# Kernel tuning notes

Hardware: AMD Instinct MI355X
Metric: run time of the kernel (lower is better)

## Reference

```python
import jax, jax.numpy as jnp
import numpy as np

H, A, S, P = 16, 768, 384, 128
D = A // H
B, N = 1, 768

def _ln(x, w=None, b=None, eps=1e-5):
    m = jnp.mean(x, axis=-1, keepdims=True)
    v = jnp.var(x, axis=-1, keepdims=True)
    y = (x - m) * jax.lax.rsqrt(v + eps)
    if w is not None:
        y = y * w
    if b is not None:
        y = y + b
    return y

def setup_inputs() -> dict:
    key = jax.random.key(0)
    ks = jax.random.split(key, 20)
    def rn(k, shape, scale=0.02):
        return jax.random.normal(k, shape, dtype=jnp.float32) * scale
    return {
        'a': jax.random.normal(ks[0], (B, N, A), dtype=jnp.float32),
        's': jax.random.normal(ks[1], (B, N, S), dtype=jnp.float32),
        'pair_rep': jax.random.normal(ks[2], (B, N, N, P), dtype=jnp.float32),
        'beta': jax.random.normal(ks[3], (B, N, N), dtype=jnp.float32),
        # AdaLN params (LN(a) no affine; LN(s) scale-only; sigmoid-gate Linear w/ bias; shift Linear no bias)
        'ln_s_w': jnp.ones((S,), jnp.float32),
        'gamma_w': rn(ks[4], (S, A)), 'gamma_b': jnp.zeros((A,), jnp.float32),
        'shift_w': rn(ks[5], (S, A)),
        # QKV
        'Wq': rn(ks[6], (A, H * D)), 'bq': jnp.zeros((H * D,), jnp.float32),
        'Wk': rn(ks[7], (A, H * D)),
        'Wv': rn(ks[8], (A, H * D)),
        # pair bias: LN + Linear(P -> H, no bias)
        'ln_p_w': jnp.ones((P,), jnp.float32), 'ln_p_b': jnp.zeros((P,), jnp.float32),
        'Wb': rn(ks[9], (P, H)),
        # gate
        'Wg': rn(ks[10], (A, H * D)),
        # output projections
        'Wp': rn(ks[11], (H * D, A)),
        'Wout': rn(ks[12], (S, A)), 'bout': jnp.full((A,), -2.0, jnp.float32),
    }

def reference(a, s, pair_rep, beta, ln_s_w, gamma_w, gamma_b, shift_w, Wq, bq, Wk, Wv, ln_p_w, ln_p_b, Wb, Wg, Wp, Wout, bout):
    # AdaLN(a, s)
    a_n = _ln(a)
    s_n = _ln(s, ln_s_w)
    a2 = jax.nn.sigmoid(s_n @ gamma_w + gamma_b) * a_n + s_n @ shift_w
    # QKV + gate, viewed as [B, N, H, D]
    q = (a2 @ Wq + bq).reshape(B, N, H, D)
    k = (a2 @ Wk).reshape(B, N, H, D)
    v = (a2 @ Wv).reshape(B, N, H, D)
    g = jax.nn.sigmoid((a2 @ Wg).reshape(B, N, H, D))
    # pair bias -> [B, H, N, N]
    bias = _ln(pair_rep, ln_p_w, ln_p_b) @ Wb          # [B, N, N, H]
    bias = bias + beta[..., None]
    bias = jnp.moveaxis(bias, -1, -3)                  # [B, H, N, N]
    # attention
    scores = jnp.einsum('bqhd,bkhd->bhqk', q, k) / np.sqrt(D).astype(np.float32) + bias
    attn = jax.nn.softmax(scores, axis=-1)
    o = jnp.einsum('bhqk,bkhd->bqhd', attn, v) * g     # [B, N, H, D]
    out = o.reshape(B, N, H * D) @ Wp                  # [B, N, A]
    out = jax.nn.sigmoid(s @ Wout + bout) * out
    return out
```

## Files before the change

kernel.cpp:

```cpp
#include <hip/hip_runtime.h>

#define N_ 768
#define S_ 384
#define H_ 16
#define D_ 48
#define P_ 128
#define NN_ (768*768)

typedef __attribute__((ext_vector_type(8))) short bf16x8;
typedef __attribute__((ext_vector_type(4))) float f32x4;

__device__ __forceinline__ unsigned short f2bf(float x) {
  unsigned int u = __float_as_uint(x);
  u = (u + 0x7fffu + ((u >> 16) & 1u)) >> 16;
  return (unsigned short)u;
}
__device__ __forceinline__ float bf2f(unsigned short h) {
  return __uint_as_float(((unsigned int)h) << 16);
}
__device__ __forceinline__ float sigm(float x) { return 1.f / (1.f + __expf(-x)); }

__global__ __launch_bounds__(256) void k_ln_prep(
    const float* __restrict__ a, const float* __restrict__ s,
    const float* __restrict__ ln_s_w, const float* __restrict__ bq,
    const float* __restrict__ ln_p_w, const float* __restrict__ ln_p_b,
    const float* __restrict__ Wb,
    float* __restrict__ a_n,
    unsigned short* __restrict__ s_n_hi, unsigned short* __restrict__ s_n_lo,
    unsigned short* __restrict__ s_hi, unsigned short* __restrict__ s_lo,
    float* __restrict__ bq4, float* __restrict__ Wprime, float* __restrict__ c12)
{
  int b = blockIdx.x;
  int t = threadIdx.x;
  if (b == N_) {
    for (int j = t; j < 3072; j += 256) bq4[j] = (j < 768) ? bq[j] : 0.f;
    for (int idx = t; idx < 2048; idx += 256) Wprime[idx] = ln_p_w[idx >> 4] * Wb[idx];
    if (t < 16) {
      float c1 = 0.f, c2 = 0.f;
      for (int p = 0; p < 128; ++p) { float wb = Wb[p*16 + t]; c1 += ln_p_w[p]*wb; c2 += ln_p_b[p]*wb; }
      c12[t] = c1; c12[16+t] = c2;
    }
    return;
  }
  __shared__ float red[16];
  int w = t >> 6, l = t & 63;
  float v0 = a[b*N_ + t], v1 = a[b*N_ + 256 + t], v2 = a[b*N_ + 512 + t];
  float sm = v0+v1+v2, sq = v0*v0 + v1*v1 + v2*v2;
  #pragma unroll
  for (int o = 32; o; o >>= 1) { sm += __shfl_xor(sm, o); sq += __shfl_xor(sq, o); }
  if (l == 0) { red[w] = sm; red[8+w] = sq; }
  __syncthreads();
  float Sa = red[0]+red[1]+red[2]+red[3];
  float Qa = red[8]+red[9]+red[10]+red[11];
  float mean = Sa * (1.f/768.f);
  float var  = Qa * (1.f/768.f) - mean*mean;
  float inv  = rsqrtf(var + 1e-5f);
  a_n[b*N_ + t]       = (v0-mean)*inv;
  a_n[b*N_ + 256 + t] = (v1-mean)*inv;
  a_n[b*N_ + 512 + t] = (v2-mean)*inv;
  __syncthreads();
  float u0 = s[b*S_ + t];
  float u1 = (t < 128) ? s[b*S_ + 256 + t] : 0.f;
  float sm2 = u0+u1, sq2 = u0*u0 + u1*u1;
  #pragma unroll
  for (int o = 32; o; o >>= 1) { sm2 += __shfl_xor(sm2, o); sq2 += __shfl_xor(sq2, o); }
  if (l == 0) { red[w] = sm2; red[8+w] = sq2; }
  __syncthreads();
  float Ss = red[0]+red[1]+red[2]+red[3];
  float Qs = red[8]+red[9]+red[10]+red[11];
  float means = Ss * (1.f/384.f);
  float vars  = Qs * (1.f/384.f) - means*means;
  float invs  = rsqrtf(vars + 1e-5f);
  {
    float sn = (u0 - means)*invs*ln_s_w[t];
    unsigned short h = f2bf(sn); s_n_hi[b*S_+t] = h; s_n_lo[b*S_+t] = f2bf(sn - bf2f(h));
    unsigned short hr = f2bf(u0); s_hi[b*S_+t] = hr; s_lo[b*S_+t] = f2bf(u0 - bf2f(hr));
  }
  if (t < 128) {
    int c = 256 + t;
    float sn = (u1 - means)*invs*ln_s_w[c];
    unsigned short h = f2bf(sn); s_n_hi[b*S_+c] = h; s_n_lo[b*S_+c] = f2bf(sn - bf2f(h));
    unsigned short hr = f2bf(u1); s_hi[b*S_+c] = hr; s_lo[b*S_+c] = f2bf(u1 - bf2f(hr));
  }
}

struct TDesc { const float* src; unsigned short* hi; unsigned short* lo; int R; int C; };
struct TArgs { TDesc d[8]; };
__global__ __launch_bounds__(256) void k_transpose(TArgs args)
{
  TDesc dd = args.d[blockIdx.z];
  int c0 = blockIdx.x * 32, r0 = blockIdx.y * 32;
  if (r0 >= dd.R || c0 >= dd.C) return;
  __shared__ float tile[32][33];
  int tx = threadIdx.x & 31, ty = threadIdx.x >> 5;
  #pragma unroll
  for (int p = 0; p < 4; ++p) {
    int r = ty + p*8;
    tile[r][tx] = dd.src[(r0 + r)*dd.C + c0 + tx];
  }
  __syncthreads();
  #pragma unroll
  for (int p = 0; p < 4; ++p) {
    int r = ty + p*8;
    float x = tile[tx][r];
    unsigned short h = f2bf(x);
    int oidx = (c0 + r)*dd.R + r0 + tx;
    dd.hi[oidx] = h; dd.lo[oidx] = f2bf(x - bf2f(h));
  }
}

__global__ __launch_bounds__(256) void k_pair_bias(
    const float* __restrict__ pair, const float* __restrict__ beta,
    const float* __restrict__ Wprime, const float* __restrict__ c12,
    float* __restrict__ bias3)
{
  __shared__ float xbuf[4][128];
  int b = blockIdx.x;
  int i = b >> 1, j0 = (b & 1) * 384;
  int t = threadIdx.x, w = t >> 6, l = t & 63;
  int h = l & 15, pg = l >> 4;
  float wreg[32];
  #pragma unroll
  for (int e = 0; e < 32; ++e) wreg[e] = Wprime[(pg*32 + e)*16 + h];
  float c1 = c12[h], c2 = c12[16 + h];
  for (int j = j0 + w; j < j0 + 384; j += 4) {
    const float* px = pair + ((long)i*N_ + j)*P_;
    float2 x2 = *(const float2*)(px + 2*l);
    *(float2*)&xbuf[w][2*l] = x2;
    float sm = x2.x + x2.y, sq = x2.x*x2.x + x2.y*x2.y;
    #pragma unroll
    for (int o = 32; o; o >>= 1) { sm += __shfl_xor(sm, o); sq += __shfl_xor(sq, o); }
    float mean = sm * (1.f/128.f);
    float var  = sq * (1.f/128.f) - mean*mean;
    float inv  = rsqrtf(var + 1e-5f);
    float acc = 0.f;
    #pragma unroll
    for (int e4 = 0; e4 < 8; ++e4) {
      float4 xv = *(const float4*)&xbuf[w][pg*32 + e4*4];
      acc = fmaf(xv.x, wreg[e4*4+0], acc);
      acc = fmaf(xv.y, wreg[e4*4+1], acc);
      acc = fmaf(xv.z, wreg[e4*4+2], acc);
      acc = fmaf(xv.w, wreg[e4*4+3], acc);
    }
    acc += __shfl_xor(acc, 16);
    acc += __shfl_xor(acc, 32);
    float outv = inv*acc - inv*mean*c1 + c2 + beta[(long)i*N_ + j];
    if (pg == 0) bias3[(long)h*NN_ + (long)i*N_ + j] = outv;
  }
}

struct GemmArgs {
  const unsigned short* Ah; const unsigned short* Al;
  const unsigned short* Bh; const unsigned short* Bl;
  int lda, ldb, K;
  long sAz, sBz;
  float* C; int ldc; long sCz;
  const float* aux0; const float* aux1;
  unsigned short* oHi; unsigned short* oLo;
  float scale;
};

template<int WTM, int WTN, bool SPLIT, int EPI>
__global__ __launch_bounds__(256) void k_gemm(GemmArgs g)
{
  constexpr int BM = 2*WTM*16, BN = 2*WTN*16;
  int z = blockIdx.z;
  int m0 = blockIdx.x * BM, n0 = blockIdx.y * BN;
  int t = threadIdx.x, l = t & 63, w = t >> 6;
  int wm = (w >> 1)*(WTM*16), wn = (w & 1)*(WTN*16);
  int r = l & 15, kg = (l >> 4)*8;
  const unsigned short* Ah = g.Ah + (long)z*g.sAz;
  const unsigned short* Bh = g.Bh + (long)z*g.sBz;
  const unsigned short* Al = nullptr; const unsigned short* Bl = nullptr;
  if constexpr (SPLIT) { Al = g.Al + (long)z*g.sAz; Bl = g.Bl + (long)z*g.sBz; }
  f32x4 acc[WTM][WTN] = {};
  for (int k0 = 0; k0 < g.K; k0 += 32) {
    bf16x8 ah[WTM], bh[WTN], al[WTM], bl[WTN];
    #pragma unroll
    for (int mt = 0; mt < WTM; ++mt) {
      long off = (long)(m0 + wm + mt*16 + r)*g.lda + k0 + kg;
      ah[mt] = *(const bf16x8*)(Ah + off);
      if constexpr (SPLIT) al[mt] = *(const bf16x8*)(Al + off);
    }
    #pragma unroll
    for (int nt = 0; nt < WTN; ++nt) {
      long off = (long)(n0 + wn + nt*16 + r)*g.ldb + k0 + kg;
      bh[nt] = *(const bf16x8*)(Bh + off);
      if constexpr (SPLIT) bl[nt] = *(const bf16x8*)(Bl + off);
    }
    #pragma unroll
    for (int mt = 0; mt < WTM; ++mt) {
      #pragma unroll
      for (int nt = 0; nt < WTN; ++nt) {
        acc[mt][nt] = __builtin_amdgcn_mfma_f32_16x16x32_bf16(ah[mt], bh[nt], acc[mt][nt], 0, 0, 0);
        if constexpr (SPLIT) {
          acc[mt][nt] = __builtin_amdgcn_mfma_f32_16x16x32_bf16(al[mt], bh[nt], acc[mt][nt], 0, 0, 0);
          acc[mt][nt] = __builtin_amdgcn_mfma_f32_16x16x32_bf16(ah[mt], bl[nt], acc[mt][nt], 0, 0, 0);
        }
      }
    }
  }
  int rb = (l >> 4)*4, cl = l & 15;
  #pragma unroll
  for (int mt = 0; mt < WTM; ++mt)
  #pragma unroll
  for (int nt = 0; nt < WTN; ++nt)
  #pragma unroll
  for (int ri = 0; ri < 4; ++ri) {
    int row = m0 + wm + mt*16 + rb + ri;
    int col = n0 + wn + nt*16 + cl;
    float v = acc[mt][nt][ri];
    if constexpr (EPI == 0) {
      g.C[(long)z*g.sCz + (long)row*g.ldc + col] = v;
    } else if constexpr (EPI == 1) {
      g.C[(long)row*g.ldc + col] = v + g.aux0[col];
    } else if constexpr (EPI == 2) {
      g.C[(long)z*g.sCz + (long)row*g.ldc + col] =
          v*g.scale + g.aux0[(long)z*NN_ + (long)row*N_ + col];
    } else if constexpr (EPI == 3) {
      if (col < D_) {
        long oidx = (long)row*N_ + z*D_ + col;
        float val = v * g.aux0[oidx];
        unsigned short hh = f2bf(val);
        g.oHi[oidx] = hh; g.oLo[oidx] = f2bf(val - bf2f(hh));
      }
    } else if constexpr (EPI == 4) {
      float sgv = sigm(v + g.aux1[col]);
      long oidx = (long)row*g.ldc + col;
      g.C[oidx] = sgv * g.aux0[oidx];
    }
  }
}

__global__ __launch_bounds__(256) void k_a2(
    const float* __restrict__ gs, const float* __restrict__ gamma_b,
    const float* __restrict__ a_n,
    unsigned short* __restrict__ a2h, unsigned short* __restrict__ a2l)
{
  int i = blockIdx.x;
  int j = blockIdx.y*256 + threadIdx.x;
  float val = sigm(gs[(long)i*1536 + j] + gamma_b[j]) * a_n[(long)i*N_ + j]
            + gs[(long)i*1536 + 768 + j];
  unsigned short h = f2bf(val);
  long idx = (long)i*N_ + j;
  a2h[idx] = h; a2l[idx] = f2bf(val - bf2f(h));
}

__global__ __launch_bounds__(256) void k_qkvg_post(
    const float* __restrict__ qkvg,
    unsigned short* __restrict__ qp, unsigned short* __restrict__ kp,
    unsigned short* __restrict__ vt, float* __restrict__ gg)
{
  int b = blockIdx.x;
  int t = threadIdx.x;
  if (b < N_) {
    long i = b;
    #pragma unroll
    for (int e = 0; e < 4; ++e) {
      int c = t + e*256;
      int h = c >> 6, d = c & 63;
      float qv = (d < D_) ? qkvg[i*3072 + h*D_ + d] : 0.f;
      float kv = (d < D_) ? qkvg[i*3072 + 768 + h*D_ + d] : 0.f;
      qp[i*1024 + c] = f2bf(qv);
      kp[i*1024 + c] = f2bf(kv);
    }
    #pragma unroll
    for (int e = 0; e < 3; ++e) {
      int c = t + e*256;
      gg[i*N_ + c] = sigm(qkvg[i*3072 + 2304 + c]);
    }
  } else {
    __shared__ float tile[64][49];
    int b2 = b - N_;
    int h = b2 / 12, i0 = (b2 % 12) * 64;
    #pragma unroll
    for (int e = 0; e < 12; ++e) {
      int idx = t + e*256;
      int il = idx / 48, d = idx % 48;
      tile[il][d] = qkvg[(long)(i0+il)*3072 + 1536 + h*D_ + d];
    }
    __syncthreads();
    #pragma unroll
    for (int e = 0; e < 12; ++e) {
      int idx = t + e*256;
      int d = idx >> 6, il = idx & 63;
      vt[(long)h*49152 + (long)d*N_ + i0 + il] = f2bf(tile[il][d]);
    }
  }
}

__global__ __launch_bounds__(256) void k_softmax(
    const float* __restrict__ scores, unsigned short* __restrict__ attn)
{
  int row = blockIdx.x*4 + (threadIdx.x >> 6);
  int l = threadIdx.x & 63;
  const float* src = scores + (long)row*N_;
  float x[12];
  #pragma unroll
  for (int e = 0; e < 12; ++e) x[e] = src[l + e*64];
  float m = x[0];
  #pragma unroll
  for (int e = 1; e < 12; ++e) m = fmaxf(m, x[e]);
  #pragma unroll
  for (int o = 32; o; o >>= 1) m = fmaxf(m, __shfl_xor(m, o));
  float ssum = 0.f;
  #pragma unroll
  for (int e = 0; e < 12; ++e) { x[e] = __expf(x[e] - m); ssum += x[e]; }
  #pragma unroll
  for (int o = 32; o; o >>= 1) ssum += __shfl_xor(ssum, o);
  float invs = 1.f / ssum;
  unsigned short* dst = attn + (long)row*N_;
  #pragma unroll
  for (int e = 0; e < 12; ++e) dst[l + e*64] = f2bf(x[e]*invs);
}

extern "C" void kernel_launch(void* const* d_in, const int* in_sizes, int n_in,
                              void* d_out, int out_size, void* d_ws, size_t ws_size,
                              hipStream_t stream) {
  const float* a      = (const float*)d_in[0];
  const float* s      = (const float*)d_in[1];
  const float* pair   = (const float*)d_in[2];
  const float* beta   = (const float*)d_in[3];
  const float* ln_s_w = (const float*)d_in[4];
  const float* gamma_w= (const float*)d_in[5];
  const float* gamma_b= (const float*)d_in[6];
  const float* shift_w= (const float*)d_in[7];
  const float* Wq     = (const float*)d_in[8];
  const float* bq     = (const float*)d_in[9];
  const float* Wk     = (const float*)d_in[10];
  const float* Wv     = (const float*)d_in[11];
  const float* ln_p_w = (const float*)d_in[12];
  const float* ln_p_b = (const float*)d_in[13];
  const float* Wb     = (const float*)d_in[14];
  const float* Wg     = (const float*)d_in[15];
  const float* Wp     = (const float*)d_in[16];
  const float* Wout   = (const float*)d_in[17];
  const float* bout   = (const float*)d_in[18];
  float* out = (float*)d_out;
  (void)in_sizes; (void)n_in; (void)out_size; (void)ws_size;

  char* ws = (char*)d_ws;
  size_t off = 0;
  auto alloc = [&](size_t bytes) -> char* {
    char* p = ws + off;
    off = (off + bytes + 255) & ~(size_t)255;
    return p;
  };
  float* bias3   = (float*)alloc((size_t)H_*NN_*4);
  float* scores  = (float*)alloc((size_t)H_*NN_*4);
  unsigned short* W4T_hi  = (unsigned short*)alloc((size_t)3072*768*2);
  unsigned short* W4T_lo  = (unsigned short*)alloc((size_t)3072*768*2);
  unsigned short* gsT_hi  = (unsigned short*)alloc((size_t)1536*384*2);
  unsigned short* gsT_lo  = (unsigned short*)alloc((size_t)1536*384*2);
  unsigned short* WpT_hi  = (unsigned short*)alloc((size_t)768*768*2);
  unsigned short* WpT_lo  = (unsigned short*)alloc((size_t)768*768*2);
  unsigned short* WoT_hi  = (unsigned short*)alloc((size_t)768*384*2);
  unsigned short* WoT_lo  = (unsigned short*)alloc((size_t)768*384*2);
  float* a_n     = (float*)alloc((size_t)N_*N_*4);
  unsigned short* s_n_hi = (unsigned short*)alloc((size_t)N_*S_*2);
  unsigned short* s_n_lo = (unsigned short*)alloc((size_t)N_*S_*2);
  unsigned short* s_hi   = (unsigned short*)alloc((size_t)N_*S_*2);
  unsigned short* s_lo   = (unsigned short*)alloc((size_t)N_*S_*2);
  float* bq4     = (float*)alloc(3072*4);
  float* Wprime  = (float*)alloc(128*16*4);
  float* c12     = (float*)alloc(32*4);
  unsigned short* a2_hi  = (unsigned short*)alloc((size_t)N_*N_*2);
  unsigned short* a2_lo  = (unsigned short*)alloc((size_t)N_*N_*2);
  float* qkvg    = (float*)alloc((size_t)N_*3072*4);
  unsigned short* qp = (unsigned short*)alloc((size_t)N_*1024*2);
  unsigned short* kp = (unsigned short*)alloc((size_t)N_*1024*2);
  unsigned short* vt = (unsigned short*)alloc((size_t)H_*64*N_*2);
  float* gate    = (float*)alloc((size_t)N_*N_*4);
  float* gs = qkvg;
  unsigned short* attn = (unsigned short*)bias3;
  unsigned short* o_hi = (unsigned short*)scores;
  unsigned short* o_lo = (unsigned short*)((char*)scores + (size_t)N_*N_*2);
  float* out1 = (float*)((char*)scores + (size_t)N_*N_*4);

  dim3 blk(256);

  k_ln_prep<<<dim3(N_ + 1), blk, 0, stream>>>(a, s, ln_s_w, bq, ln_p_w, ln_p_b, Wb,
      a_n, s_n_hi, s_n_lo, s_hi, s_lo, bq4, Wprime, c12);

  TArgs ta;
  ta.d[0] = {gamma_w, gsT_hi,               gsT_lo,               384, 768};
  ta.d[1] = {shift_w, gsT_hi + 768*384,     gsT_lo + 768*384,     384, 768};
  ta.d[2] = {Wq,      W4T_hi,               W4T_lo,               768, 768};
  ta.d[3] = {Wk,      W4T_hi + 1*768*768,   W4T_lo + 1*768*768,   768, 768};
  ta.d[4] = {Wv,      W4T_hi + 2*768*768,   W4T_lo + 2*768*768,   768, 768};
  ta.d[5] = {Wg,      W4T_hi + 3*768*768,   W4T_lo + 3*768*768,   768, 768};
  ta.d[6] = {Wp,      WpT_hi,               WpT_lo,               768, 768};
  ta.d[7] = {Wout,    WoT_hi,               WoT_lo,               384, 768};
  k_transpose<<<dim3(24, 24, 8), blk, 0, stream>>>(ta);

  k_pair_bias<<<dim3(1536), blk, 0, stream>>>(pair, beta, Wprime, c12, bias3);

  GemmArgs g1{};
  g1.Ah = s_n_hi; g1.Al = s_n_lo; g1.Bh = gsT_hi; g1.Bl = gsT_lo;
  g1.lda = 384; g1.ldb = 384; g1.K = 384; g1.C = gs; g1.ldc = 1536;
  k_gemm<4,4,true,0><<<dim3(6,12,1), blk, 0, stream>>>(g1);

  k_a2<<<dim3(768,3), blk, 0, stream>>>(gs, gamma_b, a_n, a2_hi, a2_lo);

  GemmArgs g2{};
  g2.Ah = a2_hi; g2.Al = a2_lo; g2.Bh = W4T_hi; g2.Bl = W4T_lo;
  g2.lda = 768; g2.ldb = 768; g2.K = 768; g2.C = qkvg; g2.ldc = 3072; g2.aux0 = bq4;
  k_gemm<4,4,true,1><<<dim3(6,24,1), blk, 0, stream>>>(g2);

  k_qkvg_post<<<dim3(960), blk, 0, stream>>>(qkvg, qp, kp, vt, gate);

  GemmArgs g3{};
  g3.Ah = qp; g3.Bh = kp; g3.lda = 1024; g3.ldb = 1024; g3.K = 64;
  g3.sAz = 64; g3.sBz = 64; g3.C = scores; g3.ldc = 768; g3.sCz = NN_;
  g3.aux0 = bias3; g3.scale = 0.14433756729740643f;
  k_gemm<4,4,false,2><<<dim3(6,6,16), blk, 0, stream>>>(g3);

  k_softmax<<<dim3(3072), blk, 0, stream>>>(scores, attn);

  GemmArgs g4{};
  g4.Ah = attn; g4.Bh = vt; g4.lda = 768; g4.ldb = 768; g4.K = 768;
  g4.sAz = NN_; g4.sBz = 64*768; g4.aux0 = gate; g4.oHi = o_hi; g4.oLo = o_lo;
  k_gemm<4,2,false,3><<<dim3(6,1,16), blk, 0, stream>>>(g4);

  GemmArgs g5{};
  g5.Ah = o_hi; g5.Al = o_lo; g5.Bh = WpT_hi; g5.Bl = WpT_lo;
  g5.lda = 768; g5.ldb = 768; g5.K = 768; g5.C = out1; g5.ldc = 768;
  k_gemm<4,4,true,0><<<dim3(6,6,1), blk, 0, stream>>>(g5);

  GemmArgs g6{};
  g6.Ah = s_hi; g6.Al = s_lo; g6.Bh = WoT_hi; g6.Bl = WoT_lo;
  g6.lda = 384; g6.ldb = 384; g6.K = 384; g6.C = out; g6.ldc = 768;
  g6.aux0 = out1; g6.aux1 = bout;
  k_gemm<4,4,true,4><<<dim3(6,6,1), blk, 0, stream>>>(g6);
}
```

Measured before the change: 829.7 us.

## Move pair-bias projection onto MFMA and shrink GEMM tiles for more blocks

The pair-bias kernel now computes the LayerNorm'd 128->16 projection with bf16 MFMA instructions, using a hi/lo split of both weights and activations to keep near-fp32 accuracy. This replaces the per-lane scalar FMA loop and shared-memory staging. Separately, all dense GEMM launches switch to smaller warp tiles with proportionally larger grids so more blocks fill the 256 CUs. Smaller tiles give less data reuse per block and more redundant operand loads.

```diff
diff --git a/kernel.cpp b/kernel.cpp
--- a/kernel.cpp
+++ b/kernel.cpp
@@ -19,6 +19,22 @@
   return __uint_as_float(((unsigned int)h) << 16);
 }
 __device__ __forceinline__ float sigm(float x) { return 1.f / (1.f + __expf(-x)); }
+
+__device__ __forceinline__ void split8(const float4& a, const float4& b,
+                                       bf16x8& hi, bf16x8& lo) {
+  float xs[8] = {a.x, a.y, a.z, a.w, b.x, b.y, b.z, b.w};
+  union { bf16x8 v; unsigned int u[4]; } Hh, Ll;
+  #pragma unroll
+  for (int i = 0; i < 4; ++i) {
+    unsigned int u0 = __float_as_uint(xs[2*i]);
+    unsigned int u1 = __float_as_uint(xs[2*i+1]);
+    float l0 = xs[2*i]   - __uint_as_float(u0 & 0xFFFF0000u);
+    float l1 = xs[2*i+1] - __uint_as_float(u1 & 0xFFFF0000u);
+    Hh.u[i] = (u0 >> 16) | (u1 & 0xFFFF0000u);
+    Ll.u[i] = (unsigned int)f2bf(l0) | ((unsigned int)f2bf(l1) << 16);
+  }
+  hi = Hh.v; lo = Ll.v;
+}
 
 __global__ __launch_bounds__(256) void k_ln_prep(
     const float* __restrict__ a, const float* __restrict__ s,
@@ -28,13 +44,22 @@
     float* __restrict__ a_n,
     unsigned short* __restrict__ s_n_hi, unsigned short* __restrict__ s_n_lo,
     unsigned short* __restrict__ s_hi, unsigned short* __restrict__ s_lo,
-    float* __restrict__ bq4, float* __restrict__ Wprime, float* __restrict__ c12)
+    float* __restrict__ bq4,
+    unsigned short* __restrict__ wT_hi, unsigned short* __restrict__ wT_lo,
+    float* __restrict__ c12)
 {
   int b = blockIdx.x;
   int t = threadIdx.x;
   if (b == N_) {
     for (int j = t; j < 3072; j += 256) bq4[j] = (j < 768) ? bq[j] : 0.f;
-    for (int idx = t; idx < 2048; idx += 256) Wprime[idx] = ln_p_w[idx >> 4] * Wb[idx];
+    for (int idx = t; idx < 2048; idx += 256) {
+      int p = idx & 127, h = idx >> 7;
+      float w = ln_p_w[p] * Wb[p*16 + h];
+      unsigned int u = __float_as_uint(w);
+      float lo = w - __uint_as_float(u & 0xFFFF0000u);
+      wT_hi[h*128 + p] = (unsigned short)(u >> 16);
+      wT_lo[h*128 + p] = f2bf(lo);
+    }
     if (t < 16) {
       float c1 = 0.f, c2 = 0.f;
       for (int p = 0; p < 128; ++p) { float wb = Wb[p*16 + t]; c1 += ln_p_w[p]*wb; c2 += ln_p_b[p]*wb; }
@@ -111,41 +136,57 @@
 
 __global__ __launch_bounds__(256) void k_pair_bias(
     const float* __restrict__ pair, const float* __restrict__ beta,
-    const float* __restrict__ Wprime, const float* __restrict__ c12,
-    float* __restrict__ bias3)
-{
-  __shared__ float xbuf[4][128];
-  int b = blockIdx.x;
-  int i = b >> 1, j0 = (b & 1) * 384;
-  int t = threadIdx.x, w = t >> 6, l = t & 63;
-  int h = l & 15, pg = l >> 4;
-  float wreg[32];
-  #pragma unroll
-  for (int e = 0; e < 32; ++e) wreg[e] = Wprime[(pg*32 + e)*16 + h];
-  float c1 = c12[h], c2 = c12[16 + h];
-  for (int j = j0 + w; j < j0 + 384; j += 4) {
-    const float* px = pair + ((long)i*N_ + j)*P_;
-    float2 x2 = *(const float2*)(px + 2*l);
-    *(float2*)&xbuf[w][2*l] = x2;
-    float sm = x2.x + x2.y, sq = x2.x*x2.x + x2.y*x2.y;
-    #pragma unroll
-    for (int o = 32; o; o >>= 1) { sm += __shfl_xor(sm, o); sq += __shfl_xor(sq, o); }
-    float mean = sm * (1.f/128.f);
-    float var  = sq * (1.f/128.f) - mean*mean;
-    float inv  = rsqrtf(var + 1e-5f);
-    float acc = 0.f;
-    #pragma unroll
-    for (int e4 = 0; e4 < 8; ++e4) {
-      float4 xv = *(const float4*)&xbuf[w][pg*32 + e4*4];
-      acc = fmaf(xv.x, wreg[e4*4+0], acc);
-      acc = fmaf(xv.y, wreg[e4*4+1], acc);
-      acc = fmaf(xv.z, wreg[e4*4+2], acc);
-      acc = fmaf(xv.w, wreg[e4*4+3], acc);
-    }
-    acc += __shfl_xor(acc, 16);
-    acc += __shfl_xor(acc, 32);
-    float outv = inv*acc - inv*mean*c1 + c2 + beta[(long)i*N_ + j];
-    if (pg == 0) bias3[(long)h*NN_ + (long)i*N_ + j] = outv;
+    const unsigned short* __restrict__ wT_hi, const unsigned short* __restrict__ wT_lo,
+    const float* __restrict__ c12, float* __restrict__ bias3)
+{
+  int t = threadIdx.x, l = t & 63, w = t >> 6;
+  int pos0 = blockIdx.x * 64 + w * 16;
+  int r = l & 15, kg = (l >> 4) * 8;
+  bf16x8 wh[4], wl[4];
+  #pragma unroll
+  for (int ks = 0; ks < 4; ++ks) {
+    wh[ks] = *(const bf16x8*)(wT_hi + r*128 + ks*32 + kg);
+    wl[ks] = *(const bf16x8*)(wT_lo + r*128 + ks*32 + kg);
+  }
+  const float* px = pair + (long)(pos0 + r) * 128;
+  float4 xa[4], xb[4];
+  #pragma unroll
+  for (int ks = 0; ks < 4; ++ks) {
+    xa[ks] = *(const float4*)(px + ks*32 + kg);
+    xb[ks] = *(const float4*)(px + ks*32 + kg + 4);
+  }
+  float bv = beta[pos0 + r];
+  float sm = 0.f, sq = 0.f;
+  #pragma unroll
+  for (int ks = 0; ks < 4; ++ks) {
+    sm += xa[ks].x + xa[ks].y + xa[ks].z + xa[ks].w;
+    sm += xb[ks].x + xb[ks].y + xb[ks].z + xb[ks].w;
+    sq = fmaf(xa[ks].x, xa[ks].x, sq); sq = fmaf(xa[ks].y, xa[ks].y, sq);
+    sq = fmaf(xa[ks].z, xa[ks].z, sq); sq = fmaf(xa[ks].w, xa[ks].w, sq);
+    sq = fmaf(xb[ks].x, xb[ks].x, sq); sq = fmaf(xb[ks].y, xb[ks].y, sq);
+    sq = fmaf(xb[ks].z, xb[ks].z, sq); sq = fmaf(xb[ks].w, xb[ks].w, sq);
+  }
+  sm += __shfl_xor(sm, 16); sm += __shfl_xor(sm, 32);
+  sq += __shfl_xor(sq, 16); sq += __shfl_xor(sq, 32);
+  float mean = sm * (1.f/128.f);
+  float var  = sq * (1.f/128.f) - mean*mean;
+  float inv  = rsqrtf(var + 1e-5f);
+  f32x4 acc = {};
+  #pragma unroll
+  for (int ks = 0; ks < 4; ++ks) {
+    bf16x8 xh, xl;
+    split8(xa[ks], xb[ks], xh, xl);
+    acc = __builtin_amdgcn_mfma_f32_16x16x32_bf16(wh[ks], xh, acc, 0, 0, 0);
+    acc = __builtin_amdgcn_mfma_f32_16x16x32_bf16(wl[ks], xh, acc, 0, 0, 0);
+    acc = __builtin_amdgcn_mfma_f32_16x16x32_bf16(wh[ks], xl, acc, 0, 0, 0);
+  }
+  long pos = pos0 + r;
+  int hb = (l >> 4) * 4;
+  #pragma unroll
+  for (int ri = 0; ri < 4; ++ri) {
+    int h = hb + ri;
+    float outv = inv*acc[ri] - inv*mean*c12[h] + c12[16 + h] + bv;
+    bias3[(long)h*NN_ + pos] = outv;
   }
 }
 
@@ -362,7 +403,8 @@
   unsigned short* s_hi   = (unsigned short*)alloc((size_t)N_*S_*2);
   unsigned short* s_lo   = (unsigned short*)alloc((size_t)N_*S_*2);
   float* bq4     = (float*)alloc(3072*4);
-  float* Wprime  = (float*)alloc(128*16*4);
+  unsigned short* wT_hi  = (unsigned short*)alloc(16*128*2);
+  unsigned short* wT_lo  = (unsigned short*)alloc(16*128*2);
   float* c12     = (float*)alloc(32*4);
   unsigned short* a2_hi  = (unsigned short*)alloc((size_t)N_*N_*2);
   unsigned short* a2_lo  = (unsigned short*)alloc((size_t)N_*N_*2);
@@ -380,7 +422,7 @@
   dim3 blk(256);
 
   k_ln_prep<<<dim3(N_ + 1), blk, 0, stream>>>(a, s, ln_s_w, bq, ln_p_w, ln_p_b, Wb,
-      a_n, s_n_hi, s_n_lo, s_hi, s_lo, bq4, Wprime, c12);
+      a_n, s_n_hi, s_n_lo, s_hi, s_lo, bq4, wT_hi, wT_lo, c12);
 
   TArgs ta;
   ta.d[0] = {gamma_w, gsT_hi,               gsT_lo,               384, 768};
@@ -393,19 +435,19 @@
   ta.d[7] = {Wout,    WoT_hi,               WoT_lo,               384, 768};
   k_transpose<<<dim3(24, 24, 8), blk, 0, stream>>>(ta);
 
-  k_pair_bias<<<dim3(1536), blk, 0, stream>>>(pair, beta, Wprime, c12, bias3);
+  k_pair_bias<<<dim3(NN_/64), blk, 0, stream>>>(pair, beta, wT_hi, wT_lo, c12, bias3);
 
   GemmArgs g1{};
   g1.Ah = s_n_hi; g1.Al = s_n_lo; g1.Bh = gsT_hi; g1.Bl = gsT_lo;
   g1.lda = 384; g1.ldb = 384; g1.K = 384; g1.C = gs; g1.ldc = 1536;
-  k_gemm<4,4,true,0><<<dim3(6,12,1), blk, 0, stream>>>(g1);
+  k_gemm<2,2,true,0><<<dim3(12,24,1), blk, 0, stream>>>(g1);
 
   k_a2<<<dim3(768,3), blk, 0, stream>>>(gs, gamma_b, a_n, a2_hi, a2_lo);
 
   GemmArgs g2{};
   g2.Ah = a2_hi; g2.Al = a2_lo; g2.Bh = W4T_hi; g2.Bl = W4T_lo;
   g2.lda = 768; g2.ldb = 768; g2.K = 768; g2.C = qkvg; g2.ldc = 3072; g2.aux0 = bq4;
-  k_gemm<4,4,true,1><<<dim3(6,24,1), blk, 0, stream>>>(g2);
+  k_gemm<2,2,true,1><<<dim3(12,48,1), blk, 0, stream>>>(g2);
 
   k_qkvg_post<<<dim3(960), blk, 0, stream>>>(qkvg, qp, kp, vt, gate);
 
@@ -420,16 +462,16 @@
   GemmArgs g4{};
   g4.Ah = attn; g4.Bh = vt; g4.lda = 768; g4.ldb = 768; g4.K = 768;
   g4.sAz = NN_; g4.sBz = 64*768; g4.aux0 = gate; g4.oHi = o_hi; g4.oLo = o_lo;
-  k_gemm<4,2,false,3><<<dim3(6,1,16), blk, 0, stream>>>(g4);
+  k_gemm<1,2,false,3><<<dim3(24,1,16), blk, 0, stream>>>(g4);
 
   GemmArgs g5{};
   g5.Ah = o_hi; g5.Al = o_lo; g5.Bh = WpT_hi; g5.Bl = WpT_lo;
   g5.lda = 768; g5.ldb = 768; g5.K = 768; g5.C = out1; g5.ldc = 768;
-  k_gemm<4,4,true,0><<<dim3(6,6,1), blk, 0, stream>>>(g5);
+  k_gemm<2,2,true,0><<<dim3(12,12,1), blk, 0, stream>>>(g5);
 
   GemmArgs g6{};
   g6.Ah = s_hi; g6.Al = s_lo; g6.Bh = WoT_hi; g6.Bl = WoT_lo;
   g6.lda = 384; g6.ldb = 384; g6.K = 384; g6.C = out; g6.ldc = 768;
   g6.aux0 = out1; g6.aux1 = bout;
-  k_gemm<4,4,true,4><<<dim3(6,6,1), blk, 0, stream>>>(g6);
-}
+  k_gemm<2,2,true,4><<<dim3(12,12,1), blk, 0, stream>>>(g6);
+}
```

Result: faster. 689.6 us (-16.9%).
